# Kernel optimization log

Measured on AMD Instinct MI355X. Metric: run time of the kernel, lower is better.

Reference implementation:

```python
import jax, jax.numpy as jnp
import numpy as np

D_MODEL = 1024
D_HEAD = 64


def setup_inputs() -> dict:
    key = jax.random.key(0)
    ks = jax.random.split(key, 7)
    scale = 1.0 / np.sqrt(D_MODEL)
    x = jax.random.normal(ks[0], (4, 2048, D_MODEL), dtype=jnp.float32)
    Wq = jax.random.normal(ks[1], (D_MODEL, D_HEAD), dtype=jnp.float32) * scale
    bq = jax.random.normal(ks[2], (D_HEAD,), dtype=jnp.float32) * 0.01
    Wk = jax.random.normal(ks[3], (D_MODEL, D_HEAD), dtype=jnp.float32) * scale
    bk = jax.random.normal(ks[4], (D_HEAD,), dtype=jnp.float32) * 0.01
    Wv = jax.random.normal(ks[5], (D_MODEL, D_HEAD), dtype=jnp.float32) * scale
    bv = jax.random.normal(ks[6], (D_HEAD,), dtype=jnp.float32) * 0.01
    return {"x": x, "Wq": Wq, "bq": bq, "Wk": Wk, "bk": bk, "Wv": Wv, "bv": bv}


def reference(x, Wq, bq, Wk, bk, Wv, bv):
    # x: [B, S, d_model]
    seq_len = x.shape[1]
    q = x @ Wq + bq  # [B, S, d_head]
    k = x @ Wk + bk
    v = x @ Wv + bv
    scores = jnp.einsum('bqd,bkd->bqk', q, k) * (1.0 / np.sqrt(D_HEAD))
    causal_mask = jnp.triu(jnp.ones((seq_len, seq_len), dtype=bool), k=1)
    scores = jnp.where(causal_mask, -jnp.inf, scores)
    weights = jax.nn.softmax(scores, axis=-1)  # dropout p=0.0 -> identity
    out = jnp.einsum('bqk,bkd->bqd', weights, v)  # [B, S, d_head]
    return out
```

## Files before the change

### kernel.cpp

```cpp
#include <hip/hip_runtime.h>
#include <math.h>

#define D_MODEL 1024
#define SEQ     2048
#define BATCH   4
#define NROWS   (BATCH * SEQ)

typedef short bf16x8 __attribute__((ext_vector_type(8)));
typedef float f32x4  __attribute__((ext_vector_type(4)));

static __device__ __forceinline__ unsigned short f2bf(float f) {
    unsigned int x = __float_as_uint(f);
    x += 0x7FFFu + ((x >> 16) & 1u);
    return (unsigned short)(x >> 16);
}

__global__ __launch_bounds__(256) void w_pack(
    const float* __restrict__ Wq, const float* __restrict__ Wk,
    const float* __restrict__ Wv, unsigned short* __restrict__ Wb)
{
    __shared__ float st[64][68];
    const int mat = blockIdx.x >> 4;
    const int k0  = (blockIdx.x & 15) * 64;
    const float* W = (mat == 0) ? Wq : (mat == 1) ? Wk : Wv;
    const int t  = threadIdx.x;
    const int kr = t >> 2, cs = (t & 3) * 16;
#pragma unroll
    for (int i = 0; i < 4; ++i)
        *(float4*)&st[kr][cs + i * 4] = *(const float4*)&W[(size_t)(k0 + kr) * 64 + cs + i * 4];
    __syncthreads();
    const int c = t >> 2, ks = (t & 3) * 16;
    unsigned short tmp[16];
#pragma unroll
    for (int j = 0; j < 16; ++j) tmp[j] = f2bf(st[ks + j][c]);
    *(uint4*)&Wb[(size_t)(mat * 64 + c) * D_MODEL + k0 + ks]     = *(uint4*)&tmp[0];
    *(uint4*)&Wb[(size_t)(mat * 64 + c) * D_MODEL + k0 + ks + 8] = *(uint4*)&tmp[8];
}

__global__ __launch_bounds__(192) void qkv_proj_mfma(
    const float* __restrict__ x, const unsigned short* __restrict__ Wb,
    const float* __restrict__ bq, const float* __restrict__ bk,
    const float* __restrict__ bv,
    unsigned short* __restrict__ qb, unsigned short* __restrict__ kb,
    unsigned short* __restrict__ Vt)
{
    __shared__ float stage[3][1088];

    const int tid  = threadIdx.x;
    const int wv   = tid >> 6;
    const int lane = tid & 63;
    const int lg   = lane >> 4;
    const int lc   = lane & 15;
    const int m0   = blockIdx.x * 16;
    const int n0w  = wv * 64;

    f32x4 acc[4];
#pragma unroll
    for (int nf = 0; nf < 4; ++nf) acc[nf] = (f32x4){0.f, 0.f, 0.f, 0.f};

    const float* ax = &x[(size_t)(m0 + lc) * D_MODEL + lg * 8];

#pragma unroll 4
    for (int ks = 0; ks < 32; ++ks) {
        float4 a0 = *(const float4*)(ax + ks * 32);
        float4 a1 = *(const float4*)(ax + ks * 32 + 4);
        bf16x8 af;
        af[0] = (short)f2bf(a0.x); af[1] = (short)f2bf(a0.y);
        af[2] = (short)f2bf(a0.z); af[3] = (short)f2bf(a0.w);
        af[4] = (short)f2bf(a1.x); af[5] = (short)f2bf(a1.y);
        af[6] = (short)f2bf(a1.z); af[7] = (short)f2bf(a1.w);
#pragma unroll
        for (int nf = 0; nf < 4; ++nf) {
            bf16x8 bf = *(const bf16x8*)&Wb[(size_t)(n0w + nf * 16 + lc) * D_MODEL + ks * 32 + lg * 8];
            acc[nf] = __builtin_amdgcn_mfma_f32_16x16x32_bf16(af, bf, acc[nf], 0, 0, 0);
        }
    }

    float* st = stage[wv];
    if (wv < 2) {
        const float* bias = (wv == 0) ? bq : bk;
        const float scale = (wv == 0) ? 0.125f : 1.0f;
#pragma unroll
        for (int nf = 0; nf < 4; ++nf) {
            float bs = bias[nf * 16 + lc];
#pragma unroll
            for (int r = 0; r < 4; ++r)
                st[(lg * 4 + r) * 68 + nf * 16 + lc] = (acc[nf][r] + bs) * scale;
        }
        unsigned short tmp[16];
        const int rr = lane & 15, cc0 = (lane >> 4) * 16;
#pragma unroll
        for (int j = 0; j < 16; ++j) tmp[j] = f2bf(st[rr * 68 + cc0 + j]);
        unsigned short* op = (wv == 0) ? qb : kb;
        unsigned short* dst = &op[(size_t)(m0 + rr) * 64 + cc0];
        *(uint4*)dst       = *(uint4*)&tmp[0];
        *(uint4*)(dst + 8) = *(uint4*)&tmp[8];
    } else {
#pragma unroll
        for (int nf = 0; nf < 4; ++nf) {
            float bs = bv[nf * 16 + lc];
#pragma unroll
            for (int r = 0; r < 4; ++r)
                st[(nf * 16 + lc) * 17 + lg * 4 + r] = acc[nf][r] + bs;
        }
        unsigned short tmp[16];
#pragma unroll
        for (int j = 0; j < 16; ++j) tmp[j] = f2bf(st[lane * 17 + j]);
        const int bb = m0 >> 11, seq = m0 & 2047;
        unsigned short* dst = &Vt[((size_t)(bb * 64 + lane)) * SEQ + seq];
        *(uint4*)dst       = *(uint4*)&tmp[0];
        *(uint4*)(dst + 8) = *(uint4*)&tmp[8];
    }
}

__global__ __launch_bounds__(64) void attn_partial(
    const unsigned short* __restrict__ qb, const unsigned short* __restrict__ kb,
    const unsigned short* __restrict__ Vt,
    float* __restrict__ O_part, float* __restrict__ ml)
{
    __shared__ unsigned short P_lds[16 * 72];

    const int qt = blockIdx.x;
    const int ch = blockIdx.y;
    const int b  = blockIdx.z;
    const int lane = threadIdx.x;
    const int lg = lane >> 4, lc = lane & 15;

    int nt = ((qt * 16 + 15 - ch * 512) >> 6) + 1;
    if (nt > 8) nt = 8;
    if (nt <= 0) return;

    const size_t qrow = (size_t)(b * SEQ + qt * 16 + lc);
    bf16x8 qf0 = *(const bf16x8*)&qb[qrow * 64 + lg * 8];
    bf16x8 qf1 = *(const bf16x8*)&qb[qrow * 64 + 32 + lg * 8];

    f32x4 O[4];
#pragma unroll
    for (int df = 0; df < 4; ++df) O[df] = (f32x4){0.f, 0.f, 0.f, 0.f};
    float m[4] = {-1e30f, -1e30f, -1e30f, -1e30f};
    float l[4] = {0.f, 0.f, 0.f, 0.f};

    const int rowbase = qt * 16 + lg * 4;

    bf16x8 kr[8], vr[8];
    {
        const int kb0 = ch * 512;
#pragma unroll
        for (int kf = 0; kf < 4; ++kf) {
            const unsigned short* kp = &kb[((size_t)(b * SEQ + kb0 + kf * 16 + lc)) * 64];
            kr[kf * 2]     = *(const bf16x8*)&kp[lg * 8];
            kr[kf * 2 + 1] = *(const bf16x8*)&kp[32 + lg * 8];
            const unsigned short* vp = &Vt[((size_t)(b * 64 + kf * 16 + lc)) * SEQ + kb0];
            vr[kf * 2]     = *(const bf16x8*)&vp[lg * 8];
            vr[kf * 2 + 1] = *(const bf16x8*)&vp[32 + lg * 8];
        }
    }

    for (int t = 0; t < nt; ++t) {
        const int kb0 = ch * 512 + t * 64;

        f32x4 s[4];
#pragma unroll
        for (int kf = 0; kf < 4; ++kf) {
            f32x4 z = (f32x4){0.f, 0.f, 0.f, 0.f};
            z = __builtin_amdgcn_mfma_f32_16x16x32_bf16(qf0, kr[kf * 2], z, 0, 0, 0);
            s[kf] = __builtin_amdgcn_mfma_f32_16x16x32_bf16(qf1, kr[kf * 2 + 1], z, 0, 0, 0);
        }
        if (t + 1 < nt) {
            const int kb0n = kb0 + 64;
#pragma unroll
            for (int kf = 0; kf < 4; ++kf) {
                const unsigned short* kp = &kb[((size_t)(b * SEQ + kb0n + kf * 16 + lc)) * 64];
                kr[kf * 2]     = *(const bf16x8*)&kp[lg * 8];
                kr[kf * 2 + 1] = *(const bf16x8*)&kp[32 + lg * 8];
            }
        }

#pragma unroll
        for (int r = 0; r < 4; ++r) {
            float tm = -1e30f;
#pragma unroll
            for (int kf = 0; kf < 4; ++kf) {
                float sv = s[kf][r];
                if (kb0 + kf * 16 + lc > rowbase + r) sv = -1e30f;
                s[kf][r] = sv;
                tm = fmaxf(tm, sv);
            }
            tm = fmaxf(tm, __shfl_xor(tm, 1));
            tm = fmaxf(tm, __shfl_xor(tm, 2));
            tm = fmaxf(tm, __shfl_xor(tm, 4));
            tm = fmaxf(tm, __shfl_xor(tm, 8));
            float mn  = fmaxf(m[r], tm);
            float fac = __expf(m[r] - mn);
            float ts  = 0.f;
#pragma unroll
            for (int kf = 0; kf < 4; ++kf) {
                float p = __expf(s[kf][r] - mn);
                ts += p;
                P_lds[(lg * 4 + r) * 72 + kf * 16 + lc] = f2bf(p);
            }
            ts += __shfl_xor(ts, 1);
            ts += __shfl_xor(ts, 2);
            ts += __shfl_xor(ts, 4);
            ts += __shfl_xor(ts, 8);
            l[r] = l[r] * fac + ts;
            m[r] = mn;
            O[0][r] *= fac; O[1][r] *= fac; O[2][r] *= fac; O[3][r] *= fac;
        }

        bf16x8 pf0 = *(const bf16x8*)&P_lds[lc * 72 + lg * 8];
        bf16x8 pf1 = *(const bf16x8*)&P_lds[lc * 72 + 32 + lg * 8];
#pragma unroll
        for (int df = 0; df < 4; ++df) {
            O[df] = __builtin_amdgcn_mfma_f32_16x16x32_bf16(pf0, vr[df * 2],     O[df], 0, 0, 0);
            O[df] = __builtin_amdgcn_mfma_f32_16x16x32_bf16(pf1, vr[df * 2 + 1], O[df], 0, 0, 0);
        }
        if (t + 1 < nt) {
            const int kb0n = kb0 + 64;
#pragma unroll
            for (int df = 0; df < 4; ++df) {
                const unsigned short* vp = &Vt[((size_t)(b * 64 + df * 16 + lc)) * SEQ + kb0n];
                vr[df * 2]     = *(const bf16x8*)&vp[lg * 8];
                vr[df * 2 + 1] = *(const bf16x8*)&vp[32 + lg * 8];
            }
        }
    }

    const int slot = (b * 128 + qt) * 4 + ch;
    float* Op = O_part + (size_t)slot * 1024;
#pragma unroll
    for (int df = 0; df < 4; ++df)
#pragma unroll
        for (int r = 0; r < 4; ++r)
            Op[(lg * 4 + r) * 64 + df * 16 + lc] = O[df][r];
    if (lc == 0) {
#pragma unroll
        for (int r = 0; r < 4; ++r) {
            ml[slot * 32 + lg * 4 + r]      = m[r];
            ml[slot * 32 + 16 + lg * 4 + r] = l[r];
        }
    }
}

__global__ __launch_bounds__(256) void attn_merge(
    const float* __restrict__ O_part, const float* __restrict__ ml,
    float* __restrict__ out)
{
    int idx = blockIdx.x * 256 + threadIdx.x;
    int row = idx >> 5;
    int d0  = (idx & 31) * 2;
    int b = row >> 11, seq = row & 2047;
    int qt = seq >> 4, rl = seq & 15;
    int nc = ((qt * 16 + 15) >> 9) + 1;
    int sb = (b * 128 + qt) * 4;

    float M = -1e30f;
    for (int c = 0; c < nc; ++c) M = fmaxf(M, ml[(sb + c) * 32 + rl]);
    float L = 0.f, o0 = 0.f, o1 = 0.f;
    for (int c = 0; c < nc; ++c) {
        float e = __expf(ml[(sb + c) * 32 + rl] - M);
        L += e * ml[(sb + c) * 32 + 16 + rl];
        const float* Op = O_part + (size_t)(sb + c) * 1024 + rl * 64 + d0;
        o0 += e * Op[0];
        o1 += e * Op[1];
    }
    float inv = 1.f / L;
    *(float2*)&out[(size_t)row * 64 + d0] = make_float2(o0 * inv, o1 * inv);
}

extern "C" void kernel_launch(void* const* d_in, const int* in_sizes, int n_in,
                              void* d_out, int out_size, void* d_ws, size_t ws_size,
                              hipStream_t stream)
{
    (void)in_sizes; (void)n_in; (void)out_size; (void)ws_size;

    const float* x  = (const float*)d_in[0];
    const float* Wq = (const float*)d_in[1];
    const float* bq = (const float*)d_in[2];
    const float* Wk = (const float*)d_in[3];
    const float* bk = (const float*)d_in[4];
    const float* Wv = (const float*)d_in[5];
    const float* bv = (const float*)d_in[6];
    float* out = (float*)d_out;

    char* ws = (char*)d_ws;
    unsigned short* Wb = (unsigned short*)(ws);
    unsigned short* qb = (unsigned short*)(ws + 393216);
    unsigned short* kb = (unsigned short*)(ws + 393216 + 1048576);
    unsigned short* Vt = (unsigned short*)(ws + 393216 + 2 * 1048576);
    float*          ml = (float*)(ws + 393216 + 3 * 1048576);
    float*      O_part = (float*)(ws + 393216 + 3 * 1048576 + 262144);

    w_pack<<<48, 256, 0, stream>>>(Wq, Wk, Wv, Wb);
    qkv_proj_mfma<<<512, 192, 0, stream>>>(x, Wb, bq, bk, bv, qb, kb, Vt);
    attn_partial<<<dim3(128, 4, 4), 64, 0, stream>>>(qb, kb, Vt, O_part, ml);
    attn_merge<<<1024, 256, 0, stream>>>(O_part, ml, out);
}
```

Measured before the change: 162.0 us.

## Retile QKV projection GEMM with LDS staging and register prefetch

The QKV projection kernel moves from 16-row blocks, where each wave read its own x fragments and weights straight from global memory, to a 64x96 block tile. A and B tiles are staged in LDS and shared by a 2x2 wave grid, and the next k-slice is prefetched into registers while the current one is computed. The goal is more reuse of x and weights and fewer redundant global loads, at the cost of 128x2 blocks instead of 512 and extra barriers. The epilogue is rewritten so that column splits that straddle the K and V outputs land in the right place. The attention kernel also gets a launch-bounds occupancy hint.

```diff
diff --git a/kernel.cpp b/kernel.cpp
--- a/kernel.cpp
+++ b/kernel.cpp
@@ -37,83 +37,154 @@
     *(uint4*)&Wb[(size_t)(mat * 64 + c) * D_MODEL + k0 + ks + 8] = *(uint4*)&tmp[8];
 }
 
-__global__ __launch_bounds__(192) void qkv_proj_mfma(
+__global__ __launch_bounds__(256, 1) void qkv_proj_mfma(
     const float* __restrict__ x, const unsigned short* __restrict__ Wb,
     const float* __restrict__ bq, const float* __restrict__ bk,
     const float* __restrict__ bv,
     unsigned short* __restrict__ qb, unsigned short* __restrict__ kb,
     unsigned short* __restrict__ Vt)
 {
-    __shared__ float stage[3][1088];
+    __shared__ float smem[6400];
+    unsigned short* A_lds = (unsigned short*)smem;
+    unsigned short* B_lds = A_lds + 64 * 72;
 
     const int tid  = threadIdx.x;
-    const int wv   = tid >> 6;
+    const int wid  = tid >> 6;
     const int lane = tid & 63;
+    const int wr   = wid >> 1;
+    const int wc   = wid & 1;
     const int lg   = lane >> 4;
     const int lc   = lane & 15;
-    const int m0   = blockIdx.x * 16;
-    const int n0w  = wv * 64;
-
-    f32x4 acc[4];
-#pragma unroll
-    for (int nf = 0; nf < 4; ++nf) acc[nf] = (f32x4){0.f, 0.f, 0.f, 0.f};
-
-    const float* ax = &x[(size_t)(m0 + lc) * D_MODEL + lg * 8];
-
-#pragma unroll 4
-    for (int ks = 0; ks < 32; ++ks) {
-        float4 a0 = *(const float4*)(ax + ks * 32);
-        float4 a1 = *(const float4*)(ax + ks * 32 + 4);
-        bf16x8 af;
-        af[0] = (short)f2bf(a0.x); af[1] = (short)f2bf(a0.y);
-        af[2] = (short)f2bf(a0.z); af[3] = (short)f2bf(a0.w);
-        af[4] = (short)f2bf(a1.x); af[5] = (short)f2bf(a1.y);
-        af[6] = (short)f2bf(a1.z); af[7] = (short)f2bf(a1.w);
-#pragma unroll
-        for (int nf = 0; nf < 4; ++nf) {
-            bf16x8 bf = *(const bf16x8*)&Wb[(size_t)(n0w + nf * 16 + lc) * D_MODEL + ks * 32 + lg * 8];
-            acc[nf] = __builtin_amdgcn_mfma_f32_16x16x32_bf16(af, bf, acc[nf], 0, 0, 0);
-        }
-    }
-
-    float* st = stage[wv];
-    if (wv < 2) {
-        const float* bias = (wv == 0) ? bq : bk;
-        const float scale = (wv == 0) ? 0.125f : 1.0f;
-#pragma unroll
-        for (int nf = 0; nf < 4; ++nf) {
-            float bs = bias[nf * 16 + lc];
+    const int m0   = blockIdx.x * 64;
+    const int n0   = blockIdx.y * 96;
+    const int by   = blockIdx.y;
+
+    f32x4 acc[2][3];
+#pragma unroll
+    for (int mf = 0; mf < 2; ++mf)
+#pragma unroll
+        for (int nf = 0; nf < 3; ++nf) acc[mf][nf] = (f32x4){0.f, 0.f, 0.f, 0.f};
+
+    const int arow0 = tid >> 3, ac8 = tid & 7;
+    const int brow0 = tid >> 3, bc8 = tid & 7;
+
+    float4 a0[2], a1[2];
+    uint4  brg[3];
+
+    {
+#pragma unroll
+        for (int i = 0; i < 2; ++i) {
+            const float* ap = &x[(size_t)(m0 + arow0 + 32 * i) * D_MODEL + ac8 * 8];
+            a0[i] = *(const float4*)ap;
+            a1[i] = *(const float4*)(ap + 4);
+        }
+#pragma unroll
+        for (int i = 0; i < 3; ++i)
+            brg[i] = *(const uint4*)&Wb[(size_t)(n0 + brow0 + 32 * i) * D_MODEL + bc8 * 8];
+    }
+
+    for (int it = 0; it < 16; ++it) {
+        __syncthreads();
+#pragma unroll
+        for (int i = 0; i < 2; ++i) {
+            unsigned int w0 = f2bf(a0[i].x) | ((unsigned)f2bf(a0[i].y) << 16);
+            unsigned int w1 = f2bf(a0[i].z) | ((unsigned)f2bf(a0[i].w) << 16);
+            unsigned int w2 = f2bf(a1[i].x) | ((unsigned)f2bf(a1[i].y) << 16);
+            unsigned int w3 = f2bf(a1[i].z) | ((unsigned)f2bf(a1[i].w) << 16);
+            *(uint4*)&A_lds[(arow0 + 32 * i) * 72 + ac8 * 8] = make_uint4(w0, w1, w2, w3);
+        }
+#pragma unroll
+        for (int i = 0; i < 3; ++i)
+            *(uint4*)&B_lds[(brow0 + 32 * i) * 72 + bc8 * 8] = brg[i];
+        __syncthreads();
+
+        if (it < 15) {
+            const int k0 = (it + 1) * 64;
+#pragma unroll
+            for (int i = 0; i < 2; ++i) {
+                const float* ap = &x[(size_t)(m0 + arow0 + 32 * i) * D_MODEL + k0 + ac8 * 8];
+                a0[i] = *(const float4*)ap;
+                a1[i] = *(const float4*)(ap + 4);
+            }
+#pragma unroll
+            for (int i = 0; i < 3; ++i)
+                brg[i] = *(const uint4*)&Wb[(size_t)(n0 + brow0 + 32 * i) * D_MODEL + k0 + bc8 * 8];
+        }
+
+#pragma unroll
+        for (int kk = 0; kk < 2; ++kk) {
+            bf16x8 af[2], bfr[3];
+#pragma unroll
+            for (int mf = 0; mf < 2; ++mf)
+                af[mf] = *(const bf16x8*)&A_lds[(wr * 32 + mf * 16 + lc) * 72 + kk * 32 + lg * 8];
+#pragma unroll
+            for (int nf = 0; nf < 3; ++nf)
+                bfr[nf] = *(const bf16x8*)&B_lds[(wc * 48 + nf * 16 + lc) * 72 + kk * 32 + lg * 8];
+#pragma unroll
+            for (int mf = 0; mf < 2; ++mf)
+#pragma unroll
+                for (int nf = 0; nf < 3; ++nf)
+                    acc[mf][nf] = __builtin_amdgcn_mfma_f32_16x16x32_bf16(
+                        af[mf], bfr[nf], acc[mf][nf], 0, 0, 0);
+        }
+    }
+
+    __syncthreads();
+    float* st = smem;
+#pragma unroll
+    for (int mf = 0; mf < 2; ++mf)
+#pragma unroll
+        for (int nf = 0; nf < 3; ++nf)
 #pragma unroll
             for (int r = 0; r < 4; ++r)
-                st[(lg * 4 + r) * 68 + nf * 16 + lc] = (acc[nf][r] + bs) * scale;
-        }
-        unsigned short tmp[16];
-        const int rr = lane & 15, cc0 = (lane >> 4) * 16;
-#pragma unroll
-        for (int j = 0; j < 16; ++j) tmp[j] = f2bf(st[rr * 68 + cc0 + j]);
-        unsigned short* op = (wv == 0) ? qb : kb;
-        unsigned short* dst = &op[(size_t)(m0 + rr) * 64 + cc0];
-        *(uint4*)dst       = *(uint4*)&tmp[0];
-        *(uint4*)(dst + 8) = *(uint4*)&tmp[8];
+                st[(wr * 32 + mf * 16 + lg * 4 + r) * 100 + wc * 48 + nf * 16 + lc] = acc[mf][nf][r];
+    __syncthreads();
+
+    unsigned short tmp[16];
+    if (by == 0) {
+        {
+            const int row = tid >> 2, c16 = (tid & 3) * 16;
+#pragma unroll
+            for (int j = 0; j < 16; ++j)
+                tmp[j] = f2bf((st[row * 100 + c16 + j] + bq[c16 + j]) * 0.125f);
+            unsigned short* dst = &qb[(size_t)(m0 + row) * 64 + c16];
+            *(uint4*)dst       = *(uint4*)&tmp[0];
+            *(uint4*)(dst + 8) = *(uint4*)&tmp[8];
+        }
+        if (tid < 128) {
+            const int row = tid >> 1, c16 = (tid & 1) * 16;
+#pragma unroll
+            for (int j = 0; j < 16; ++j)
+                tmp[j] = f2bf(st[row * 100 + 64 + c16 + j] + bk[c16 + j]);
+            unsigned short* dst = &kb[(size_t)(m0 + row) * 64 + c16];
+            *(uint4*)dst       = *(uint4*)&tmp[0];
+            *(uint4*)(dst + 8) = *(uint4*)&tmp[8];
+        }
     } else {
-#pragma unroll
-        for (int nf = 0; nf < 4; ++nf) {
-            float bs = bv[nf * 16 + lc];
-#pragma unroll
-            for (int r = 0; r < 4; ++r)
-                st[(nf * 16 + lc) * 17 + lg * 4 + r] = acc[nf][r] + bs;
-        }
-        unsigned short tmp[16];
-#pragma unroll
-        for (int j = 0; j < 16; ++j) tmp[j] = f2bf(st[lane * 17 + j]);
-        const int bb = m0 >> 11, seq = m0 & 2047;
-        unsigned short* dst = &Vt[((size_t)(bb * 64 + lane)) * SEQ + seq];
-        *(uint4*)dst       = *(uint4*)&tmp[0];
-        *(uint4*)(dst + 8) = *(uint4*)&tmp[8];
-    }
-}
-
-__global__ __launch_bounds__(64) void attn_partial(
+        if (tid < 128) {
+            const int row = tid >> 1, c16 = (tid & 1) * 16;
+#pragma unroll
+            for (int j = 0; j < 16; ++j)
+                tmp[j] = f2bf(st[row * 100 + c16 + j] + bk[32 + c16 + j]);
+            unsigned short* dst = &kb[(size_t)(m0 + row) * 64 + 32 + c16];
+            *(uint4*)dst       = *(uint4*)&tmp[0];
+            *(uint4*)(dst + 8) = *(uint4*)&tmp[8];
+        }
+        {
+            const int d = tid >> 2, s16 = (tid & 3) * 16;
+            const float bs = bv[d];
+#pragma unroll
+            for (int j = 0; j < 16; ++j)
+                tmp[j] = f2bf(st[(s16 + j) * 100 + 32 + d] + bs);
+            const int bb = m0 >> 11, seq0 = m0 & 2047;
+            unsigned short* dst = &Vt[((size_t)(bb * 64 + d)) * SEQ + seq0 + s16];
+            *(uint4*)dst       = *(uint4*)&tmp[0];
+            *(uint4*)(dst + 8) = *(uint4*)&tmp[8];
+        }
+    }
+}
+
+__global__ __launch_bounds__(64, 2) void attn_partial(
     const unsigned short* __restrict__ qb, const unsigned short* __restrict__ kb,
     const unsigned short* __restrict__ Vt,
     float* __restrict__ O_part, float* __restrict__ ml)
@@ -292,7 +363,7 @@
     float*      O_part = (float*)(ws + 393216 + 3 * 1048576 + 262144);
 
     w_pack<<<48, 256, 0, stream>>>(Wq, Wk, Wv, Wb);
-    qkv_proj_mfma<<<512, 192, 0, stream>>>(x, Wb, bq, bk, bv, qb, kb, Vt);
+    qkv_proj_mfma<<<dim3(128, 2), 256, 0, stream>>>(x, Wb, bq, bk, bv, qb, kb, Vt);
     attn_partial<<<dim3(128, 4, 4), 64, 0, stream>>>(qb, kb, Vt, O_part, ml);
     attn_merge<<<1024, 256, 0, stream>>>(O_part, ml, out);
 }
```

Measured after the change: 140.6 us. 1.15x faster.
